# Performance work log

Measured on AMD Instinct MI355X. Metric: run time of the kernel, lower is better.

Reference implementation:

```python
import jax, jax.numpy as jnp
import numpy as np

N_NODES = 20000
N_EDGES = 640000
IN_DIM, HID_DIM, OUT_DIM = 128, 128, 64


def setup_inputs() -> dict:
    key = jax.random.key(0)
    k = jax.random.split(key, 6)
    x = jax.random.normal(k[0], (N_NODES, IN_DIM), dtype=jnp.float32)
    edge_index = jax.random.randint(k[1], (2, N_EDGES), 0, N_NODES, dtype=jnp.int64)
    W1 = jax.random.normal(k[2], (IN_DIM, HID_DIM), dtype=jnp.float32) * (1.0 / np.sqrt(IN_DIM))
    b1 = jnp.zeros((HID_DIM,), dtype=jnp.float32)
    W2 = jax.random.normal(k[3], (HID_DIM, OUT_DIM), dtype=jnp.float32) * (1.0 / np.sqrt(HID_DIM))
    b2 = jnp.zeros((OUT_DIM,), dtype=jnp.float32)
    return {"x": x, "edge_index": edge_index, "W1": W1, "b1": b1, "W2": W2, "b2": b2}


def _gcn_conv(h, W, b, src, dst, n_nodes):
    # h' = D^-1/2 (A + I) D^-1/2 (h W) + b   (PyG GCNConv with self-loops)
    h = h @ W                                              # [N, F_out]
    ones = jnp.ones((src.shape[0],), dtype=h.dtype)
    deg = jax.ops.segment_sum(ones, dst, num_segments=n_nodes) + 1.0  # +1 for self-loop
    dinv = jax.lax.rsqrt(deg)                              # [N]
    w = dinv[src] * dinv[dst]                              # per-edge norm [E]
    msg = h[src] * w[:, None]                              # gather + scale [E, F_out]
    agg = jax.ops.segment_sum(msg, dst, num_segments=n_nodes)  # scatter-add [N, F_out]
    # self-loop contribution: norm_ii = dinv[i]^2
    return agg + h * (dinv * dinv)[:, None] + b


def reference(x, edge_index, W1, b1, W2, b2):
    src, dst = edge_index[0], edge_index[1]
    n = x.shape[0]
    h = _gcn_conv(x, W1, b1, src, dst, n)
    h = jax.nn.relu(h)
    # dropout is identity in eval mode (training=False)
    out = _gcn_conv(h, W2, b2, src, dst, n)
    return out
```

## Files before the change

### kernel.cpp

```cpp
#include <hip/hip_runtime.h>


#define N_NODES 20000
#define N_EDGES 640000
#define IN_DIM 128
#define HID_DIM 128
#define OUT_DIM 64

#define STRIDE 80
#define SCAT_NB (N_EDGES / 256)
#define WT_NB ((128 * 128 + 64 * 128) / 256)
#define GEMM1_NB ((2 * (N_NODES / 16) + 3) / 4)
#define AGG_NB ((N_NODES + 3) / 4)

typedef _Float16 half8_t __attribute__((ext_vector_type(8)));
typedef float float4_t __attribute__((ext_vector_type(4)));

__global__ __launch_bounds__(256) void k_build(const int* __restrict__ src,
                                               const int* __restrict__ dst,
                                               int* __restrict__ cnt,
                                               unsigned short* __restrict__ esrc_pad,
                                               const float* __restrict__ W1,
                                               const float* __restrict__ W2,
                                               _Float16* __restrict__ WT1,
                                               _Float16* __restrict__ WT2) {
    const int b = blockIdx.x, tid = threadIdx.x;
    if (b < SCAT_NB) {
        const int e = b * 256 + tid;
        const int s = __builtin_nontemporal_load(&src[e]);
        const int d = __builtin_nontemporal_load(&dst[e]);
        unsigned int rank = atomicAdd((unsigned int*)&cnt[d], 1u);
        if (rank < STRIDE) esrc_pad[d * STRIDE + rank] = (unsigned short)s;
    } else {
        int i = (b - SCAT_NB) * 256 + tid;
        if (i < 128 * 128) {
            int c = i >> 7, k = i & 127;
            WT1[i] = (_Float16)W1[k * 128 + c];
        } else {
            int o = i - 128 * 128;
            int c = o >> 7, k = o & 127;
            WT2[o] = (_Float16)W2[k * 64 + c];
        }
    }
}

__global__ __launch_bounds__(256) void k_g1(const float* __restrict__ A,
                                            const _Float16* __restrict__ WT,
                                            const int* __restrict__ cnt,
                                            _Float16* __restrict__ GA,
                                            _Float16* __restrict__ GB) {
    const int wave = threadIdx.x >> 6;
    const int lane = threadIdx.x & 63;
    const int task = blockIdx.x * 4 + wave;
    if (task >= 2 * (N_NODES / 16)) return;
    const int strip = task >> 1;
    const int nh = task & 1;
    const int row0 = strip * 16;
    const int mrow = row0 + (lane & 15);
    const int kq = (lane >> 4) * 8;
    _Float16* G = nh ? GB : GA;

    half8_t af[4];
#pragma unroll
    for (int kc = 0; kc < 4; ++kc) {
        const float* ap = A + (size_t)mrow * 128 + kc * 32 + kq;
        float4_t f0 = __builtin_nontemporal_load((const float4_t*)ap);
        float4_t f1 = __builtin_nontemporal_load((const float4_t*)(ap + 4));
        half8_t h;
        h[0] = (_Float16)f0[0]; h[1] = (_Float16)f0[1];
        h[2] = (_Float16)f0[2]; h[3] = (_Float16)f0[3];
        h[4] = (_Float16)f1[0]; h[5] = (_Float16)f1[1];
        h[6] = (_Float16)f1[2]; h[7] = (_Float16)f1[3];
        af[kc] = h;
    }

    float4_t acc[4];
#pragma unroll
    for (int nt = 0; nt < 4; ++nt) acc[nt] = (float4_t)(0.0f);
#pragma unroll
    for (int nt = 0; nt < 4; ++nt) {
        const _Float16* wp = WT + (size_t)((nh * 4 + nt) * 16 + (lane & 15)) * 128 + kq;
#pragma unroll
        for (int kc = 0; kc < 4; ++kc) {
            half8_t bf = *(const half8_t*)(wp + kc * 32);
            acc[nt] = __builtin_amdgcn_mfma_f32_16x16x32_f16(af[kc], bf, acc[nt], 0, 0, 0);
        }
    }
#pragma unroll
    for (int r = 0; r < 4; ++r) {
        int row = row0 + (lane >> 4) * 4 + r;
        float dv = rsqrtf((float)cnt[row] + 1.0f);
#pragma unroll
        for (int nt = 0; nt < 4; ++nt)
            G[(size_t)row * 64 + nt * 16 + (lane & 15)] = (_Float16)(dv * acc[nt][r]);
    }
}

__global__ __launch_bounds__(256) void k_mgemm2(const _Float16* __restrict__ A,
                                                const _Float16* __restrict__ WT,
                                                const int* __restrict__ cnt,
                                                _Float16* __restrict__ G) {
    const int wave = threadIdx.x >> 6;
    const int lane = threadIdx.x & 63;
    const int task = blockIdx.x * 4 + wave;
    if (task >= 2 * (N_NODES / 16)) return;
    const int strip = task >> 1;
    const int nh = task & 1;
    const int row0 = strip * 16;
    const int mrow = row0 + (lane & 15);
    const int kq = (lane >> 4) * 8;

    half8_t af[4];
#pragma unroll
    for (int kc = 0; kc < 4; ++kc)
        af[kc] = __builtin_nontemporal_load(
            (const half8_t*)(A + (size_t)mrow * 128 + kc * 32 + kq));

    float4_t acc[2];
#pragma unroll
    for (int nt = 0; nt < 2; ++nt) acc[nt] = (float4_t)(0.0f);
#pragma unroll
    for (int nt = 0; nt < 2; ++nt) {
        const _Float16* wp = WT + (size_t)((nh * 2 + nt) * 16 + (lane & 15)) * 128 + kq;
#pragma unroll
        for (int kc = 0; kc < 4; ++kc) {
            half8_t bf = *(const half8_t*)(wp + kc * 32);
            acc[nt] = __builtin_amdgcn_mfma_f32_16x16x32_f16(af[kc], bf, acc[nt], 0, 0, 0);
        }
    }
#pragma unroll
    for (int r = 0; r < 4; ++r) {
        int row = row0 + (lane >> 4) * 4 + r;
        float dv = rsqrtf((float)cnt[row] + 1.0f);
#pragma unroll
        for (int nt = 0; nt < 2; ++nt)
            G[(size_t)row * 64 + (nh * 2 + nt) * 16 + (lane & 15)] =
                (_Float16)(dv * acc[nt][r]);
    }
}

__global__ __launch_bounds__(256) void k_agg128f(const int* __restrict__ cnt,
                                                 const unsigned short* __restrict__ esrc_pad,
                                                 const _Float16* __restrict__ Ga,
                                                 const _Float16* __restrict__ Gb,
                                                 const float* __restrict__ bias,
                                                 _Float16* __restrict__ out) {
    const int half = (blockIdx.x >= AGG_NB) ? 1 : 0;
    const int bb = blockIdx.x - half * AGG_NB;
    const int wave = threadIdx.x >> 6;
    const int lane = threadIdx.x & 63;
    const int node = bb * 4 + wave;
    if (node >= N_NODES) return;
    const _Float16* __restrict__ G = half ? Gb : Ga;
    const int COL0 = half << 6;
    const int eidx = lane >> 3;
    const int flane = lane & 7;

    const int end = cnt[node];
    const int base = node * STRIDE;

    float acc[8];
#pragma unroll
    for (int p = 0; p < 8; ++p) acc[p] = 0.0f;
    if (lane < 8) {
        half8_t s = *(const half8_t*)(G + (size_t)node * 64 + flane * 8);
#pragma unroll
        for (int p = 0; p < 8; ++p) acc[p] = (float)s[p];
    }

    int j = 0;
    for (; j + 15 < end; j += 16) {
        int s0 = (int)__builtin_nontemporal_load(&esrc_pad[base + j + eidx]);
        int s1 = (int)__builtin_nontemporal_load(&esrc_pad[base + j + 8 + eidx]);
        half8_t r0 = *(const half8_t*)(G + (size_t)s0 * 64 + flane * 8);
        half8_t r1 = *(const half8_t*)(G + (size_t)s1 * 64 + flane * 8);
#pragma unroll
        for (int p = 0; p < 8; ++p) acc[p] += (float)r0[p] + (float)r1[p];
    }
    for (; j + 7 < end; j += 8) {
        int s = (int)__builtin_nontemporal_load(&esrc_pad[base + j + eidx]);
        half8_t r = *(const half8_t*)(G + (size_t)s * 64 + flane * 8);
#pragma unroll
        for (int p = 0; p < 8; ++p) acc[p] += (float)r[p];
    }
    if (j < end) {
        int idx = j + eidx;
        int s = (int)__builtin_nontemporal_load(
            &esrc_pad[base + ((idx < end) ? idx : (end - 1))]);
        float valid = (idx < end) ? 1.0f : 0.0f;
        half8_t r = *(const half8_t*)(G + (size_t)s * 64 + flane * 8);
#pragma unroll
        for (int p = 0; p < 8; ++p) acc[p] += valid * (float)r[p];
    }

#pragma unroll
    for (int p = 0; p < 8; ++p) {
        acc[p] += __shfl_xor(acc[p], 32, 64);
        acc[p] += __shfl_xor(acc[p], 16, 64);
        acc[p] += __shfl_xor(acc[p], 8, 64);
    }

    if (lane < 8) {
        float dv = rsqrtf((float)end + 1.0f);
        float4_t b0 = *(const float4_t*)(bias + COL0 + flane * 8);
        float4_t b1 = *(const float4_t*)(bias + COL0 + flane * 8 + 4);
        half8_t o;
        o[0] = (_Float16)fmaxf(acc[0] * dv + b0[0], 0.0f);
        o[1] = (_Float16)fmaxf(acc[1] * dv + b0[1], 0.0f);
        o[2] = (_Float16)fmaxf(acc[2] * dv + b0[2], 0.0f);
        o[3] = (_Float16)fmaxf(acc[3] * dv + b0[3], 0.0f);
        o[4] = (_Float16)fmaxf(acc[4] * dv + b1[0], 0.0f);
        o[5] = (_Float16)fmaxf(acc[5] * dv + b1[1], 0.0f);
        o[6] = (_Float16)fmaxf(acc[6] * dv + b1[2], 0.0f);
        o[7] = (_Float16)fmaxf(acc[7] * dv + b1[3], 0.0f);
        __builtin_nontemporal_store(
            o, (half8_t*)(out + (size_t)node * 128 + COL0 + flane * 8));
    }
}

__global__ __launch_bounds__(256) void k_agg64(const int* __restrict__ cnt,
                                               const unsigned short* __restrict__ esrc_pad,
                                               const _Float16* __restrict__ g,
                                               const float* __restrict__ bias,
                                               float* __restrict__ out) {
    const int wave = threadIdx.x >> 6;
    const int lane = threadIdx.x & 63;
    const int node = blockIdx.x * 4 + wave;
    if (node >= N_NODES) return;
    const int eidx = lane >> 3;
    const int flane = lane & 7;

    const int end = cnt[node];
    const int base = node * STRIDE;

    float acc[8];
#pragma unroll
    for (int p = 0; p < 8; ++p) acc[p] = 0.0f;
    if (lane < 8) {
        half8_t s = *(const half8_t*)(g + (size_t)node * 64 + flane * 8);
#pragma unroll
        for (int p = 0; p < 8; ++p) acc[p] = (float)s[p];
    }

    int j = 0;
    for (; j + 15 < end; j += 16) {
        int s0 = (int)__builtin_nontemporal_load(&esrc_pad[base + j + eidx]);
        int s1 = (int)__builtin_nontemporal_load(&esrc_pad[base + j + 8 + eidx]);
        half8_t r0 = *(const half8_t*)(g + (size_t)s0 * 64 + flane * 8);
        half8_t r1 = *(const half8_t*)(g + (size_t)s1 * 64 + flane * 8);
#pragma unroll
        for (int p = 0; p < 8; ++p) acc[p] += (float)r0[p] + (float)r1[p];
    }
    for (; j + 7 < end; j += 8) {
        int s = (int)__builtin_nontemporal_load(&esrc_pad[base + j + eidx]);
        half8_t r = *(const half8_t*)(g + (size_t)s * 64 + flane * 8);
#pragma unroll
        for (int p = 0; p < 8; ++p) acc[p] += (float)r[p];
    }
    if (j < end) {
        int idx = j + eidx;
        int s = (int)__builtin_nontemporal_load(
            &esrc_pad[base + ((idx < end) ? idx : (end - 1))]);
        float valid = (idx < end) ? 1.0f : 0.0f;
        half8_t r = *(const half8_t*)(g + (size_t)s * 64 + flane * 8);
#pragma unroll
        for (int p = 0; p < 8; ++p) acc[p] += valid * (float)r[p];
    }

#pragma unroll
    for (int p = 0; p < 8; ++p) {
        acc[p] += __shfl_xor(acc[p], 32, 64);
        acc[p] += __shfl_xor(acc[p], 16, 64);
        acc[p] += __shfl_xor(acc[p], 8, 64);
    }

    if (lane < 8) {
        float dv = rsqrtf((float)end + 1.0f);
        float4_t b0 = *(const float4_t*)(bias + flane * 8);
        float4_t b1 = *(const float4_t*)(bias + flane * 8 + 4);
        float4_t o0, o1;
        o0[0] = acc[0] * dv + b0[0]; o0[1] = acc[1] * dv + b0[1];
        o0[2] = acc[2] * dv + b0[2]; o0[3] = acc[3] * dv + b0[3];
        o1[0] = acc[4] * dv + b1[0]; o1[1] = acc[5] * dv + b1[1];
        o1[2] = acc[6] * dv + b1[2]; o1[3] = acc[7] * dv + b1[3];
        __builtin_nontemporal_store(o0, (float4_t*)(out + (size_t)node * 64 + flane * 8));
        __builtin_nontemporal_store(o1, (float4_t*)(out + (size_t)node * 64 + flane * 8 + 4));
    }
}

extern "C" void kernel_launch(void* const* d_in, const int* in_sizes, int n_in,
                              void* d_out, int out_size, void* d_ws, size_t ws_size,
                              hipStream_t stream) {
    const float* x  = (const float*)d_in[0];
    const int*   ei = (const int*)d_in[1];
    const float* W1 = (const float*)d_in[2];
    const float* b1 = (const float*)d_in[3];
    const float* W2 = (const float*)d_in[4];
    const float* b2 = (const float*)d_in[5];

    const int* src = ei;
    const int* dst = ei + N_EDGES;

    char* w = (char*)d_ws;
    unsigned short* esrc_pad = (unsigned short*)w; w += sizeof(unsigned short) * (size_t)N_NODES * STRIDE;
    _Float16*       g1a      = (_Float16*)w;       w += sizeof(_Float16) * (size_t)N_NODES * 64;
    _Float16*       g1b      = (_Float16*)w;       w += sizeof(_Float16) * (size_t)N_NODES * 64;
    _Float16*       h1p      = (_Float16*)w;       w += sizeof(_Float16) * (size_t)N_NODES * HID_DIM;
    _Float16*       g2       = (_Float16*)w;       w += sizeof(_Float16) * (size_t)N_NODES * OUT_DIM;
    _Float16*       WT1      = (_Float16*)w;       w += sizeof(_Float16) * 128 * 128;
    _Float16*       WT2      = (_Float16*)w;       w += sizeof(_Float16) * 64 * 128;
    int*            cnt      = (int*)w;            w += sizeof(int) * N_NODES;
    float*          out      = (float*)d_out;

    hipMemsetAsync(cnt, 0, sizeof(int) * N_NODES, stream);
    k_build<<<SCAT_NB + WT_NB, 256, 0, stream>>>(src, dst, cnt, esrc_pad, W1, W2, WT1, WT2);

    k_g1<<<GEMM1_NB, 256, 0, stream>>>(x, WT1, cnt, g1a, g1b);
    k_agg128f<<<2 * AGG_NB, 256, 0, stream>>>(cnt, esrc_pad, g1a, g1b, b1, h1p);

    k_mgemm2<<<GEMM1_NB, 256, 0, stream>>>(h1p, WT2, cnt, g2);
    k_agg64<<<AGG_NB, 256, 0, stream>>>(cnt, esrc_pad, g2, b2, out);
}
```

Measured before the change: 163.2 us.

## Fuse GCN stages: merge scatter with GEMM1, fuse layer-1 aggregation with GEMM2

The memset is replaced by a small pre-kernel that zeroes the degree counts and transposes the weights. The edge scatter and the first GEMM now run as one launch, so the GEMM no longer waits on the degree counts. Source-side normalisation moves into the aggregation, which reads each neighbour's degree per edge. The layer-1 aggregation plus ReLU writes into LDS and feeds the second GEMM in the same block, removing the h1 round trip through global memory and two launches. The cost is an extra per-edge cnt gather and rsqrt, and lower parallelism in the fused mid kernel, which runs 16 rows per block with a serial loop over 4 nodes per wave.

After: 165.9 us. Within noise of the previous version (+1.6%).

```diff
diff --git a/kernel.cpp b/kernel.cpp
--- a/kernel.cpp
+++ b/kernel.cpp
@@ -9,21 +9,40 @@
 
 #define STRIDE 80
 #define SCAT_NB (N_EDGES / 256)
-#define WT_NB ((128 * 128 + 64 * 128) / 256)
-#define GEMM1_NB ((2 * (N_NODES / 16) + 3) / 4)
-#define AGG_NB ((N_NODES + 3) / 4)
+#define G1_NB 625
+#define G1_TASKS (2 * (N_NODES / 16))
+#define PRE_ITEMS (128 * 128 + 64 * 128 + N_NODES)
+#define PRE_NB ((PRE_ITEMS + 255) / 256)
 
 typedef _Float16 half8_t __attribute__((ext_vector_type(8)));
 typedef float float4_t __attribute__((ext_vector_type(4)));
 
-__global__ __launch_bounds__(256) void k_build(const int* __restrict__ src,
+__global__ __launch_bounds__(256) void k_pre(const float* __restrict__ W1,
+                                             const float* __restrict__ W2,
+                                             _Float16* __restrict__ WT1,
+                                             _Float16* __restrict__ WT2,
+                                             int* __restrict__ cnt) {
+    int i = blockIdx.x * 256 + threadIdx.x;
+    if (i < 128 * 128) {
+        int c = i >> 7, k = i & 127;
+        WT1[i] = (_Float16)W1[k * 128 + c];
+    } else if (i < 128 * 128 + 64 * 128) {
+        int o = i - 128 * 128;
+        int c = o >> 7, k = o & 127;
+        WT2[o] = (_Float16)W2[k * 64 + c];
+    } else {
+        int n = i - (128 * 128 + 64 * 128);
+        if (n < N_NODES) cnt[n] = 0;
+    }
+}
+
+__global__ __launch_bounds__(256) void k_front(const int* __restrict__ src,
                                                const int* __restrict__ dst,
                                                int* __restrict__ cnt,
                                                unsigned short* __restrict__ esrc_pad,
-                                               const float* __restrict__ W1,
-                                               const float* __restrict__ W2,
-                                               _Float16* __restrict__ WT1,
-                                               _Float16* __restrict__ WT2) {
+                                               const _Float16* __restrict__ WT1,
+                                               const float* __restrict__ x,
+                                               _Float16* __restrict__ G) {
     const int b = blockIdx.x, tid = threadIdx.x;
     if (b < SCAT_NB) {
         const int e = b * 256 + tid;
@@ -31,39 +50,22 @@
         const int d = __builtin_nontemporal_load(&dst[e]);
         unsigned int rank = atomicAdd((unsigned int*)&cnt[d], 1u);
         if (rank < STRIDE) esrc_pad[d * STRIDE + rank] = (unsigned short)s;
-    } else {
-        int i = (b - SCAT_NB) * 256 + tid;
-        if (i < 128 * 128) {
-            int c = i >> 7, k = i & 127;
-            WT1[i] = (_Float16)W1[k * 128 + c];
-        } else {
-            int o = i - 128 * 128;
-            int c = o >> 7, k = o & 127;
-            WT2[o] = (_Float16)W2[k * 64 + c];
-        }
-    }
-}
-
-__global__ __launch_bounds__(256) void k_g1(const float* __restrict__ A,
-                                            const _Float16* __restrict__ WT,
-                                            const int* __restrict__ cnt,
-                                            _Float16* __restrict__ GA,
-                                            _Float16* __restrict__ GB) {
-    const int wave = threadIdx.x >> 6;
-    const int lane = threadIdx.x & 63;
-    const int task = blockIdx.x * 4 + wave;
-    if (task >= 2 * (N_NODES / 16)) return;
+        return;
+    }
+    const int wave = tid >> 6;
+    const int lane = tid & 63;
+    const int task = (b - SCAT_NB) * 4 + wave;
+    if (task >= G1_TASKS) return;
     const int strip = task >> 1;
     const int nh = task & 1;
     const int row0 = strip * 16;
     const int mrow = row0 + (lane & 15);
     const int kq = (lane >> 4) * 8;
-    _Float16* G = nh ? GB : GA;
 
     half8_t af[4];
 #pragma unroll
     for (int kc = 0; kc < 4; ++kc) {
-        const float* ap = A + (size_t)mrow * 128 + kc * 32 + kq;
+        const float* ap = x + (size_t)mrow * 128 + kc * 32 + kq;
         float4_t f0 = __builtin_nontemporal_load((const float4_t*)ap);
         float4_t f1 = __builtin_nontemporal_load((const float4_t*)(ap + 4));
         half8_t h;
@@ -73,13 +75,12 @@
         h[6] = (_Float16)f1[2]; h[7] = (_Float16)f1[3];
         af[kc] = h;
     }
-
     float4_t acc[4];
 #pragma unroll
     for (int nt = 0; nt < 4; ++nt) acc[nt] = (float4_t)(0.0f);
 #pragma unroll
     for (int nt = 0; nt < 4; ++nt) {
-        const _Float16* wp = WT + (size_t)((nh * 4 + nt) * 16 + (lane & 15)) * 128 + kq;
+        const _Float16* wp = WT1 + (size_t)((nh * 4 + nt) * 16 + (lane & 15)) * 128 + kq;
 #pragma unroll
         for (int kc = 0; kc < 4; ++kc) {
             half8_t bf = *(const half8_t*)(wp + kc * 32);
@@ -89,108 +90,166 @@
 #pragma unroll
     for (int r = 0; r < 4; ++r) {
         int row = row0 + (lane >> 4) * 4 + r;
-        float dv = rsqrtf((float)cnt[row] + 1.0f);
 #pragma unroll
         for (int nt = 0; nt < 4; ++nt)
-            G[(size_t)row * 64 + nt * 16 + (lane & 15)] = (_Float16)(dv * acc[nt][r]);
-    }
-}
-
-__global__ __launch_bounds__(256) void k_mgemm2(const _Float16* __restrict__ A,
-                                                const _Float16* __restrict__ WT,
-                                                const int* __restrict__ cnt,
-                                                _Float16* __restrict__ G) {
+            G[(size_t)row * 128 + nh * 64 + nt * 16 + (lane & 15)] =
+                (_Float16)acc[nt][r];
+    }
+}
+
+__global__ __launch_bounds__(256) void k_mid(const int* __restrict__ cnt,
+                                             const unsigned short* __restrict__ esrc_pad,
+                                             const _Float16* __restrict__ G,
+                                             const _Float16* __restrict__ WT2,
+                                             const float* __restrict__ b1,
+                                             _Float16* __restrict__ g2) {
+    __shared__ _Float16 h1[16][136];
+    const int tid = threadIdx.x;
+    const int wave = tid >> 6;
+    const int lane = tid & 63;
+    const int row0 = blockIdx.x * 16;
+    const int eidx = lane >> 4;
+    const int fl = lane & 15;
+
+    for (int r4 = 0; r4 < 4; ++r4) {
+        const int rr = wave * 4 + r4;
+        const int node = row0 + rr;
+        const int end = cnt[node];
+        const float dvd = rsqrtf((float)end + 1.0f);
+        const int base = node * STRIDE;
+
+        float acc[8];
+#pragma unroll
+        for (int p = 0; p < 8; ++p) acc[p] = 0.0f;
+        if (eidx == 0) {
+            half8_t sv = *(const half8_t*)(G + (size_t)node * 128 + fl * 8);
+#pragma unroll
+            for (int p = 0; p < 8; ++p) acc[p] = dvd * (float)sv[p];
+        }
+        int j = 0;
+        for (; j + 7 < end; j += 8) {
+            int s0 = (int)__builtin_nontemporal_load(&esrc_pad[base + j + eidx]);
+            int s1 = (int)__builtin_nontemporal_load(&esrc_pad[base + j + 4 + eidx]);
+            float dv0 = rsqrtf((float)cnt[s0] + 1.0f);
+            float dv1 = rsqrtf((float)cnt[s1] + 1.0f);
+            half8_t r0 = *(const half8_t*)(G + (size_t)s0 * 128 + fl * 8);
+            half8_t r1 = *(const half8_t*)(G + (size_t)s1 * 128 + fl * 8);
+#pragma unroll
+            for (int p = 0; p < 8; ++p)
+                acc[p] += dv0 * (float)r0[p] + dv1 * (float)r1[p];
+        }
+        for (; j + 3 < end; j += 4) {
+            int s = (int)__builtin_nontemporal_load(&esrc_pad[base + j + eidx]);
+            float dvs = rsqrtf((float)cnt[s] + 1.0f);
+            half8_t r = *(const half8_t*)(G + (size_t)s * 128 + fl * 8);
+#pragma unroll
+            for (int p = 0; p < 8; ++p) acc[p] += dvs * (float)r[p];
+        }
+        if (j < end) {
+            int idx = j + eidx;
+            int s = (int)__builtin_nontemporal_load(
+                &esrc_pad[base + ((idx < end) ? idx : (end - 1))]);
+            float valid = (idx < end) ? 1.0f : 0.0f;
+            float dvs = rsqrtf((float)cnt[s] + 1.0f);
+            half8_t r = *(const half8_t*)(G + (size_t)s * 128 + fl * 8);
+#pragma unroll
+            for (int p = 0; p < 8; ++p) acc[p] += valid * dvs * (float)r[p];
+        }
+#pragma unroll
+        for (int p = 0; p < 8; ++p) {
+            acc[p] += __shfl_xor(acc[p], 16, 64);
+            acc[p] += __shfl_xor(acc[p], 32, 64);
+        }
+        if (eidx == 0) {
+            float4_t c0 = *(const float4_t*)(b1 + fl * 8);
+            float4_t c1 = *(const float4_t*)(b1 + fl * 8 + 4);
+            half8_t o;
+            o[0] = (_Float16)fmaxf(acc[0] * dvd + c0[0], 0.0f);
+            o[1] = (_Float16)fmaxf(acc[1] * dvd + c0[1], 0.0f);
+            o[2] = (_Float16)fmaxf(acc[2] * dvd + c0[2], 0.0f);
+            o[3] = (_Float16)fmaxf(acc[3] * dvd + c0[3], 0.0f);
+            o[4] = (_Float16)fmaxf(acc[4] * dvd + c1[0], 0.0f);
+            o[5] = (_Float16)fmaxf(acc[5] * dvd + c1[1], 0.0f);
+            o[6] = (_Float16)fmaxf(acc[6] * dvd + c1[2], 0.0f);
+            o[7] = (_Float16)fmaxf(acc[7] * dvd + c1[3], 0.0f);
+            *(half8_t*)&h1[rr][fl * 8] = o;
+        }
+    }
+    __syncthreads();
+
+    const int fr = lane & 15;
+    const int kq = (lane >> 4) * 8;
+    half8_t af[4];
+#pragma unroll
+    for (int kc = 0; kc < 4; ++kc)
+        af[kc] = *(const half8_t*)&h1[fr][kc * 32 + kq];
+    float4_t acc2 = (float4_t)(0.0f);
+    const _Float16* wp = WT2 + (size_t)(wave * 16 + fr) * 128 + kq;
+#pragma unroll
+    for (int kc = 0; kc < 4; ++kc) {
+        half8_t bf = *(const half8_t*)(wp + kc * 32);
+        acc2 = __builtin_amdgcn_mfma_f32_16x16x32_f16(af[kc], bf, acc2, 0, 0, 0);
+    }
+#pragma unroll
+    for (int r = 0; r < 4; ++r) {
+        int row = row0 + (lane >> 4) * 4 + r;
+        g2[(size_t)row * 64 + wave * 16 + fr] = (_Float16)acc2[r];
+    }
+}
+
+__global__ __launch_bounds__(256) void k_back(const int* __restrict__ cnt,
+                                              const unsigned short* __restrict__ esrc_pad,
+                                              const _Float16* __restrict__ g2,
+                                              const float* __restrict__ b2,
+                                              float* __restrict__ out) {
     const int wave = threadIdx.x >> 6;
     const int lane = threadIdx.x & 63;
-    const int task = blockIdx.x * 4 + wave;
-    if (task >= 2 * (N_NODES / 16)) return;
-    const int strip = task >> 1;
-    const int nh = task & 1;
-    const int row0 = strip * 16;
-    const int mrow = row0 + (lane & 15);
-    const int kq = (lane >> 4) * 8;
-
-    half8_t af[4];
-#pragma unroll
-    for (int kc = 0; kc < 4; ++kc)
-        af[kc] = __builtin_nontemporal_load(
-            (const half8_t*)(A + (size_t)mrow * 128 + kc * 32 + kq));
-
-    float4_t acc[2];
-#pragma unroll
-    for (int nt = 0; nt < 2; ++nt) acc[nt] = (float4_t)(0.0f);
-#pragma unroll
-    for (int nt = 0; nt < 2; ++nt) {
-        const _Float16* wp = WT + (size_t)((nh * 2 + nt) * 16 + (lane & 15)) * 128 + kq;
-#pragma unroll
-        for (int kc = 0; kc < 4; ++kc) {
-            half8_t bf = *(const half8_t*)(wp + kc * 32);
-            acc[nt] = __builtin_amdgcn_mfma_f32_16x16x32_f16(af[kc], bf, acc[nt], 0, 0, 0);
-        }
-    }
-#pragma unroll
-    for (int r = 0; r < 4; ++r) {
-        int row = row0 + (lane >> 4) * 4 + r;
-        float dv = rsqrtf((float)cnt[row] + 1.0f);
-#pragma unroll
-        for (int nt = 0; nt < 2; ++nt)
-            G[(size_t)row * 64 + (nh * 2 + nt) * 16 + (lane & 15)] =
-                (_Float16)(dv * acc[nt][r]);
-    }
-}
-
-__global__ __launch_bounds__(256) void k_agg128f(const int* __restrict__ cnt,
-                                                 const unsigned short* __restrict__ esrc_pad,
-                                                 const _Float16* __restrict__ Ga,
-                                                 const _Float16* __restrict__ Gb,
-                                                 const float* __restrict__ bias,
-                                                 _Float16* __restrict__ out) {
-    const int half = (blockIdx.x >= AGG_NB) ? 1 : 0;
-    const int bb = blockIdx.x - half * AGG_NB;
-    const int wave = threadIdx.x >> 6;
-    const int lane = threadIdx.x & 63;
-    const int node = bb * 4 + wave;
+    const int node = blockIdx.x * 4 + wave;
     if (node >= N_NODES) return;
-    const _Float16* __restrict__ G = half ? Gb : Ga;
-    const int COL0 = half << 6;
     const int eidx = lane >> 3;
-    const int flane = lane & 7;
+    const int fl = lane & 7;
 
     const int end = cnt[node];
+    const float dvd = rsqrtf((float)end + 1.0f);
     const int base = node * STRIDE;
 
     float acc[8];
 #pragma unroll
     for (int p = 0; p < 8; ++p) acc[p] = 0.0f;
     if (lane < 8) {
-        half8_t s = *(const half8_t*)(G + (size_t)node * 64 + flane * 8);
-#pragma unroll
-        for (int p = 0; p < 8; ++p) acc[p] = (float)s[p];
+        half8_t s = *(const half8_t*)(g2 + (size_t)node * 64 + fl * 8);
+#pragma unroll
+        for (int p = 0; p < 8; ++p) acc[p] = dvd * (float)s[p];
     }
 
     int j = 0;
     for (; j + 15 < end; j += 16) {
         int s0 = (int)__builtin_nontemporal_load(&esrc_pad[base + j + eidx]);
         int s1 = (int)__builtin_nontemporal_load(&esrc_pad[base + j + 8 + eidx]);
-        half8_t r0 = *(const half8_t*)(G + (size_t)s0 * 64 + flane * 8);
-        half8_t r1 = *(const half8_t*)(G + (size_t)s1 * 64 + flane * 8);
-#pragma unroll
-        for (int p = 0; p < 8; ++p) acc[p] += (float)r0[p] + (float)r1[p];
+        float dv0 = rsqrtf((float)cnt[s0] + 1.0f);
+        float dv1 = rsqrtf((float)cnt[s1] + 1.0f);
+        half8_t r0 = *(const half8_t*)(g2 + (size_t)s0 * 64 + fl * 8);
+        half8_t r1 = *(const half8_t*)(g2 + (size_t)s1 * 64 + fl * 8);
+#pragma unroll
+        for (int p = 0; p < 8; ++p)
+            acc[p] += dv0 * (float)r0[p] + dv1 * (float)r1[p];
     }
     for (; j + 7 < end; j += 8) {
         int s = (int)__builtin_nontemporal_load(&esrc_pad[base + j + eidx]);
-        half8_t r = *(const half8_t*)(G + (size_t)s * 64 + flane * 8);
-#pragma unroll
-        for (int p = 0; p < 8; ++p) acc[p] += (float)r[p];
+        float dvs = rsqrtf((float)cnt[s] + 1.0f);
+        half8_t r = *(const half8_t*)(g2 + (size_t)s * 64 + fl * 8);
+#pragma unroll
+        for (int p = 0; p < 8; ++p) acc[p] += dvs * (float)r[p];
     }
     if (j < end) {
         int idx = j + eidx;
         int s = (int)__builtin_nontemporal_load(
             &esrc_pad[base + ((idx < end) ? idx : (end - 1))]);
         float valid = (idx < end) ? 1.0f : 0.0f;
-        half8_t r = *(const half8_t*)(G + (size_t)s * 64 + flane * 8);
-#pragma unroll
-        for (int p = 0; p < 8; ++p) acc[p] += valid * (float)r[p];
+        float dvs = rsqrtf((float)cnt[s] + 1.0f);
+        half8_t r = *(const half8_t*)(g2 + (size_t)s * 64 + fl * 8);
+#pragma unroll
+        for (int p = 0; p < 8; ++p) acc[p] += valid * dvs * (float)r[p];
     }
 
 #pragma unroll
@@ -201,90 +260,15 @@
     }
 
     if (lane < 8) {
-        float dv = rsqrtf((float)end + 1.0f);
-        float4_t b0 = *(const float4_t*)(bias + COL0 + flane * 8);
-        float4_t b1 = *(const float4_t*)(bias + COL0 + flane * 8 + 4);
-        half8_t o;
-        o[0] = (_Float16)fmaxf(acc[0] * dv + b0[0], 0.0f);
-        o[1] = (_Float16)fmaxf(acc[1] * dv + b0[1], 0.0f);
-        o[2] = (_Float16)fmaxf(acc[2] * dv + b0[2], 0.0f);
-        o[3] = (_Float16)fmaxf(acc[3] * dv + b0[3], 0.0f);
-        o[4] = (_Float16)fmaxf(acc[4] * dv + b1[0], 0.0f);
-        o[5] = (_Float16)fmaxf(acc[5] * dv + b1[1], 0.0f);
-        o[6] = (_Float16)fmaxf(acc[6] * dv + b1[2], 0.0f);
-        o[7] = (_Float16)fmaxf(acc[7] * dv + b1[3], 0.0f);
-        __builtin_nontemporal_store(
-            o, (half8_t*)(out + (size_t)node * 128 + COL0 + flane * 8));
-    }
-}
-
-__global__ __launch_bounds__(256) void k_agg64(const int* __restrict__ cnt,
-                                               const unsigned short* __restrict__ esrc_pad,
-                                               const _Float16* __restrict__ g,
-                                               const float* __restrict__ bias,
-                                               float* __restrict__ out) {
-    const int wave = threadIdx.x >> 6;
-    const int lane = threadIdx.x & 63;
-    const int node = blockIdx.x * 4 + wave;
-    if (node >= N_NODES) return;
-    const int eidx = lane >> 3;
-    const int flane = lane & 7;
-
-    const int end = cnt[node];
-    const int base = node * STRIDE;
-
-    float acc[8];
-#pragma unroll
-    for (int p = 0; p < 8; ++p) acc[p] = 0.0f;
-    if (lane < 8) {
-        half8_t s = *(const half8_t*)(g + (size_t)node * 64 + flane * 8);
-#pragma unroll
-        for (int p = 0; p < 8; ++p) acc[p] = (float)s[p];
-    }
-
-    int j = 0;
-    for (; j + 15 < end; j += 16) {
-        int s0 = (int)__builtin_nontemporal_load(&esrc_pad[base + j + eidx]);
-        int s1 = (int)__builtin_nontemporal_load(&esrc_pad[base + j + 8 + eidx]);
-        half8_t r0 = *(const half8_t*)(g + (size_t)s0 * 64 + flane * 8);
-        half8_t r1 = *(const half8_t*)(g + (size_t)s1 * 64 + flane * 8);
-#pragma unroll
-        for (int p = 0; p < 8; ++p) acc[p] += (float)r0[p] + (float)r1[p];
-    }
-    for (; j + 7 < end; j += 8) {
-        int s = (int)__builtin_nontemporal_load(&esrc_pad[base + j + eidx]);
-        half8_t r = *(const half8_t*)(g + (size_t)s * 64 + flane * 8);
-#pragma unroll
-        for (int p = 0; p < 8; ++p) acc[p] += (float)r[p];
-    }
-    if (j < end) {
-        int idx = j + eidx;
-        int s = (int)__builtin_nontemporal_load(
-            &esrc_pad[base + ((idx < end) ? idx : (end - 1))]);
-        float valid = (idx < end) ? 1.0f : 0.0f;
-        half8_t r = *(const half8_t*)(g + (size_t)s * 64 + flane * 8);
-#pragma unroll
-        for (int p = 0; p < 8; ++p) acc[p] += valid * (float)r[p];
-    }
-
-#pragma unroll
-    for (int p = 0; p < 8; ++p) {
-        acc[p] += __shfl_xor(acc[p], 32, 64);
-        acc[p] += __shfl_xor(acc[p], 16, 64);
-        acc[p] += __shfl_xor(acc[p], 8, 64);
-    }
-
-    if (lane < 8) {
-        float dv = rsqrtf((float)end + 1.0f);
-        float4_t b0 = *(const float4_t*)(bias + flane * 8);
-        float4_t b1 = *(const float4_t*)(bias + flane * 8 + 4);
+        float4_t c0 = *(const float4_t*)(b2 + fl * 8);
+        float4_t c1 = *(const float4_t*)(b2 + fl * 8 + 4);
         float4_t o0, o1;
-        o0[0] = acc[0] * dv + b0[0]; o0[1] = acc[1] * dv + b0[1];
-        o0[2] = acc[2] * dv + b0[2]; o0[3] = acc[3] * dv + b0[3];
-        o1[0] = acc[4] * dv + b1[0]; o1[1] = acc[5] * dv + b1[1];
-        o1[2] = acc[6] * dv + b1[2]; o1[3] = acc[7] * dv + b1[3];
-        __builtin_nontemporal_store(o0, (float4_t*)(out + (size_t)node * 64 + flane * 8));
-        __builtin_nontemporal_store(o1, (float4_t*)(out + (size_t)node * 64 + flane * 8 + 4));
+        o0[0] = acc[0] * dvd + c0[0]; o0[1] = acc[1] * dvd + c0[1];
+        o0[2] = acc[2] * dvd + c0[2]; o0[3] = acc[3] * dvd + c0[3];
+        o1[0] = acc[4] * dvd + c1[0]; o1[1] = acc[5] * dvd + c1[1];
+        o1[2] = acc[6] * dvd + c1[2]; o1[3] = acc[7] * dvd + c1[3];
+        __builtin_nontemporal_store(o0, (float4_t*)(out + (size_t)node * 64 + fl * 8));
+        __builtin_nontemporal_store(o1, (float4_t*)(out + (size_t)node * 64 + fl * 8 + 4));
     }
 }
 
@@ -303,21 +287,15 @@
 
     char* w = (char*)d_ws;
     unsigned short* esrc_pad = (unsigned short*)w; w += sizeof(unsigned short) * (size_t)N_NODES * STRIDE;
-    _Float16*       g1a      = (_Float16*)w;       w += sizeof(_Float16) * (size_t)N_NODES * 64;
-    _Float16*       g1b      = (_Float16*)w;       w += sizeof(_Float16) * (size_t)N_NODES * 64;
-    _Float16*       h1p      = (_Float16*)w;       w += sizeof(_Float16) * (size_t)N_NODES * HID_DIM;
+    _Float16*       G        = (_Float16*)w;       w += sizeof(_Float16) * (size_t)N_NODES * 128;
     _Float16*       g2       = (_Float16*)w;       w += sizeof(_Float16) * (size_t)N_NODES * OUT_DIM;
     _Float16*       WT1      = (_Float16*)w;       w += sizeof(_Float16) * 128 * 128;
     _Float16*       WT2      = (_Float16*)w;       w += sizeof(_Float16) * 64 * 128;
     int*            cnt      = (int*)w;            w += sizeof(int) * N_NODES;
     float*          out      = (float*)d_out;
 
-    hipMemsetAsync(cnt, 0, sizeof(int) * N_NODES, stream);
-    k_build<<<SCAT_NB + WT_NB, 256, 0, stream>>>(src, dst, cnt, esrc_pad, W1, W2, WT1, WT2);
-
-    k_g1<<<GEMM1_NB, 256, 0, stream>>>(x, WT1, cnt, g1a, g1b);
-    k_agg128f<<<2 * AGG_NB, 256, 0, stream>>>(cnt, esrc_pad, g1a, g1b, b1, h1p);
-
-    k_mgemm2<<<GEMM1_NB, 256, 0, stream>>>(h1p, WT2, cnt, g2);
-    k_agg64<<<AGG_NB, 256, 0, stream>>>(cnt, esrc_pad, g2, b2, out);
-}
+    k_pre<<<PRE_NB, 256, 0, stream>>>(W1, W2, WT1, WT2, cnt);
+    k_front<<<SCAT_NB + G1_NB, 256, 0, stream>>>(src, dst, cnt, esrc_pad, WT1, x, G);
+    k_mid<<<N_NODES / 16, 256, 0, stream>>>(cnt, esrc_pad, G, WT2, b1, g2);
+    k_back<<<(N_NODES + 3) / 4, 256, 0, stream>>>(cnt, esrc_pad, g2, b2, out);
+}
```
